# Kernel optimization log

Measured on AMD Instinct MI355X. Metric: run time of the kernel, lower is better.

## Reference

```python
import jax, jax.numpy as jnp
import numpy as np

PAD_LABEL = 15
NUM_TAGS = 15


def setup_inputs() -> dict:
    key = jax.random.key(0)
    k1, k2, k3 = jax.random.split(key, 3)
    B, T, C = 4096, 512, NUM_TAGS
    logits = jax.random.normal(k1, (B, T, C), dtype=jnp.float32)
    y_true = jax.random.randint(k2, (B, T), 0, PAD_LABEL + 1, dtype=jnp.int32)
    # CRF transition matrix (learned param), glorot-ish scale
    transitions = jax.random.normal(k3, (C, C), dtype=jnp.float32) * 0.25
    return {"logits": logits, "y_true": y_true, "transitions": transitions}


def _log_norm(logits, transitions, mask):
    # logits: (B, T, C) float32, mask: (B, T) bool
    alpha0 = logits[:, 0, :]                       # (B, C)
    # scan over timesteps 1..T-1
    emits = jnp.swapaxes(logits[:, 1:, :], 0, 1)    # (T-1, B, C)
    masks = jnp.swapaxes(mask[:, 1:], 0, 1)         # (T-1, B)

    def step(alpha, inp):
        emit_t, mask_t = inp                        # (B, C), (B,)
        # scores[b, i, j] = alpha[b, i] + trans[i, j] + emit_t[b, j]
        scores = alpha[:, :, None] + transitions[None, :, :] + emit_t[:, None, :]
        new_alpha = jax.scipy.special.logsumexp(scores, axis=1)  # (B, C)
        alpha = jnp.where(mask_t[:, None], new_alpha, alpha)
        return alpha, None

    alpha, _ = jax.lax.scan(step, alpha0, (emits, masks))
    return jax.scipy.special.logsumexp(alpha, axis=1)  # (B,)


def _sequence_score(logits, transitions, labels, mask):
    mask_f = mask.astype(jnp.float32)
    safe_labels = jnp.where(mask, labels, 0)                    # (B, T)
    # emission scores along gold path
    em = jnp.take_along_axis(logits, safe_labels[:, :, None], axis=2)[:, :, 0]
    emission_score = jnp.sum(em * mask_f, axis=1)               # (B,)
    # transition scores between consecutive valid positions
    prev, curr = safe_labels[:, :-1], safe_labels[:, 1:]
    tmask_f = (mask[:, 1:] & mask[:, :-1]).astype(jnp.float32)
    trans_scores = transitions[prev, curr]                      # (B, T-1)
    transition_score = jnp.sum(trans_scores * tmask_f, axis=1)  # (B,)
    return emission_score + transition_score


def reference(logits, y_true, transitions):
    mask = y_true != PAD_LABEL                                  # (B, T) bool
    logZ = _log_norm(logits, transitions, mask)
    path_score = _sequence_score(logits, transitions, y_true, mask)
    nll = jnp.clip(logZ - path_score, 0.0, 1000000.0)
    return jnp.mean(nll)
```

## Files before the change

kernel.cpp:

```cpp
#include <hip/hip_runtime.h>

#define L2E  1.4426950408889634f
#define LN2f 0.6931471805599453f

template<int CTRL>
__device__ __forceinline__ float dppf(float x) {
  int r = __builtin_amdgcn_update_dpp(0, __builtin_bit_cast(int, x), CTRL, 0xF, 0xF, true);
  return __builtin_bit_cast(float, r);
}
template<int CTRL>
__device__ __forceinline__ int dppi(int x) {
  return __builtin_amdgcn_update_dpp(0, x, CTRL, 0xF, 0xF, true);
}

__device__ __forceinline__ float bflymax16(float x) {
  x = fmaxf(x, dppf<0xB1>(x));
  x = fmaxf(x, dppf<0x4E>(x));
  x = fmaxf(x, dppf<0x141>(x));
  x = fmaxf(x, dppf<0x140>(x));
  return x;
}

#define DOT(shv, tot) {                                   \
    float t0_ = (shv) * Wror[0], t1_ = 0.f, t2_ = 0.f, t3_ = 0.f; \
    t1_ = fmaf(dppf<0x121>(shv), Wror[1],  t1_);          \
    t2_ = fmaf(dppf<0x122>(shv), Wror[2],  t2_);          \
    t3_ = fmaf(dppf<0x123>(shv), Wror[3],  t3_);          \
    t0_ = fmaf(dppf<0x124>(shv), Wror[4],  t0_);          \
    t1_ = fmaf(dppf<0x125>(shv), Wror[5],  t1_);          \
    t2_ = fmaf(dppf<0x126>(shv), Wror[6],  t2_);          \
    t3_ = fmaf(dppf<0x127>(shv), Wror[7],  t3_);          \
    t0_ = fmaf(dppf<0x128>(shv), Wror[8],  t0_);          \
    t1_ = fmaf(dppf<0x129>(shv), Wror[9],  t1_);          \
    t2_ = fmaf(dppf<0x12A>(shv), Wror[10], t2_);          \
    t3_ = fmaf(dppf<0x12B>(shv), Wror[11], t3_);          \
    t0_ = fmaf(dppf<0x12C>(shv), Wror[12], t0_);          \
    t1_ = fmaf(dppf<0x12D>(shv), Wror[13], t1_);          \
    t2_ = fmaf(dppf<0x12E>(shv), Wror[14], t2_);          \
    t3_ = fmaf(dppf<0x12F>(shv), Wror[15], t3_);          \
    tot = (t0_ + t1_) + (t2_ + t3_); }

template<bool BWD>
__device__ __forceinline__ void scan(const float* __restrict__ ep,
                                     const int* __restrict__ ys,
                                     const float (&Wror)[16],
                                     int j, int jm,
                                     float& ownO, float& MO, float& eaccO) {
  float own, M, eacc;
  float ebuf[8]; int ybuf[8];
  if (!BWD) {
    const float a0 = ep[0];
    const int y0 = ys[0];
    eacc = (y0 == jm) ? a0 : 0.f;
    const float A = (j < 15) ? a0 * L2E : -1.0e30f;
    const float M0 = bflymax16(A);
    own = exp2f(A - M0);
    M = M0;
    #pragma unroll
    for (int i = 0; i < 8; ++i) { ebuf[i] = ep[(1 + i) * 15]; ybuf[i] = ys[1 + i]; }
  } else {
    eacc = 0.f;
    own = (j < 15) ? 1.f : 0.f;
    M = 0.f;
    #pragma unroll
    for (int i = 0; i < 8; ++i) { ebuf[i] = ep[(511 - i) * 15]; ybuf[i] = ys[511 - i]; }
  }

  if (!BWD) {
    for (int sb = 0; sb < 31; ++sb) {
      #pragma unroll
      for (int k = 0; k < 8; ++k) {
        const int t = 1 + sb * 8 + k;
        const float emit = ebuf[k]; const int yv = ybuf[k];
        const int tn = (t + 8 > 255) ? 255 : t + 8;
        ebuf[k] = ep[tn * 15]; ybuf[k] = ys[tn];
        const float p = exp2f(emit * L2E);
        float tot; DOT(own, tot);
        const float cand = tot * p;
        own = (yv != 15) ? cand : own;
        eacc += (yv == jm) ? emit : 0.f;
        if (k == 7) {
          const float m = bflymax16(own);
          own *= __builtin_amdgcn_rcpf(m);
          M += log2f(m);
        }
      }
    }
    #pragma unroll
    for (int k = 0; k < 7; ++k) {
      const float emit = ebuf[k]; const int yv = ybuf[k];
      const float p = exp2f(emit * L2E);
      float tot; DOT(own, tot);
      const float cand = tot * p;
      own = (yv != 15) ? cand : own;
      eacc += (yv == jm) ? emit : 0.f;
    }
  } else {
    for (int sb = 0; sb < 32; ++sb) {
      #pragma unroll
      for (int k = 0; k < 8; ++k) {
        const int t = 511 - (sb * 8 + k);
        const float emit = ebuf[k]; const int yv = ybuf[k];
        const int tn = (t - 8 < 256) ? 256 : t - 8;
        ebuf[k] = ep[tn * 15]; ybuf[k] = ys[tn];
        const float p = exp2f(emit * L2E);
        const float share = own * p;
        float tot; DOT(share, tot);
        own = (yv != 15) ? tot : own;
        eacc += (yv == jm) ? emit : 0.f;
        if (k == 7) {
          const float m = bflymax16(own);
          own *= __builtin_amdgcn_rcpf(m);
          M += log2f(m);
        }
      }
    }
  }
  ownO = own; MO = M; eaccO = eacc;
}

__global__ __launch_bounds__(256, 2)
void crf_rot(const float* __restrict__ logits, const int* __restrict__ yg,
             const float* __restrict__ trans, float* __restrict__ out) {
  __shared__ float Tl[240];
  __shared__ int   yl[8 * 512];
  __shared__ float comb[8][2][16];
  __shared__ float pathE[8][2];
  __shared__ float transS[8];
  __shared__ float blks[8];

  const int tid = threadIdx.x;
  if (tid < 225) Tl[tid] = trans[tid];
  {
    const int4* src = (const int4*)(yg + (size_t)blockIdx.x * 4096);
    int4* dst = (int4*)yl;
    #pragma unroll
    for (int k = 0; k < 4; ++k) dst[tid + k * 256] = src[tid + k * 256];
  }
  __syncthreads();

  {
    const int q = tid >> 5, l32 = tid & 31;
    const int* ys = yl + q * 512;
    float acc = 0.f;
    #pragma unroll
    for (int m = 0; m < 16; ++m) {
      const int t = 1 + l32 + 32 * m;
      if (t < 512) {
        const int yc = ys[t], yp = ys[t - 1];
        if (yc < 15 && yp < 15) acc += Tl[yp * 15 + yc];
      }
    }
    #pragma unroll
    for (int k = 1; k < 32; k <<= 1) acc += __shfl_xor(acc, k, 32);
    if (l32 == 0) transS[q] = acc;
  }

  const int wave = tid >> 6, lane = tid & 63;
  const int j = lane & 15;
  const int sLoc = (wave >> 1) * 4 + (lane >> 4);
  const bool isFwd = (wave & 1) == 0;
  const int seq = blockIdx.x * 8 + sLoc;
  const int jj = (j < 15) ? j : 14;
  const int jm = (j < 15) ? j : 255;
  const float* ep = logits + (size_t)seq * 7680 + jj;
  const int* ys = yl + sLoc * 512;

  float Wror[16];
  Wror[0] = (j < 15) ? exp2f(Tl[j * 16] * L2E) : 0.f;
#define SETW(R) { const int s_ = dppi<0x120 + (R)>(j);                  \
    const bool v_ = (j < 15) && (s_ < 15);                              \
    const int ix_ = isFwd ? s_ * 15 + j : j * 15 + s_;                  \
    Wror[R] = v_ ? exp2f(Tl[ix_] * L2E) : 0.f; }
  SETW(1)  SETW(2)  SETW(3)  SETW(4)  SETW(5)
  SETW(6)  SETW(7)  SETW(8)  SETW(9)  SETW(10)
  SETW(11) SETW(12) SETW(13) SETW(14) SETW(15)
#undef SETW

  float own, M, eacc;
  if (isFwd) scan<false>(ep, ys, Wror, j, jm, own, M, eacc);
  else       scan<true >(ep, ys, Wror, j, jm, own, M, eacc);

  const int dir = isFwd ? 0 : 1;
  if (j < 15) comb[sLoc][dir][j] = M + log2f(own);
  #pragma unroll
  for (int k = 1; k < 16; k <<= 1) eacc += __shfl_xor(eacc, k, 16);
  if (j == 0) pathE[sLoc][dir] = eacc;

  __syncthreads();

  if (tid < 8) {
    float mx = -3.0e38f; float s[15];
    #pragma unroll
    for (int i = 0; i < 15; ++i) {
      s[i] = comb[tid][0][i] + comb[tid][1][i];
      mx = fmaxf(mx, s[i]);
    }
    float sum = 0.f;
    #pragma unroll
    for (int i = 0; i < 15; ++i) sum += exp2f(s[i] - mx);
    const float logZ = (mx + log2f(sum)) * LN2f;
    const float path = pathE[tid][0] + pathE[tid][1] + transS[tid];
    float nll = logZ - path;
    nll = fminf(fmaxf(nll, 0.f), 1000000.f);
    blks[tid] = nll;
  }
  __syncthreads();
  if (tid == 0) {
    float tot = (blks[0] + blks[1]) + (blks[2] + blks[3]) +
                (blks[4] + blks[5]) + (blks[6] + blks[7]);
    atomicAdd(out, tot * (1.0f / 4096.0f));
  }
}

extern "C" void kernel_launch(void* const* d_in, const int* in_sizes, int n_in,
                              void* d_out, int out_size, void* d_ws, size_t ws_size,
                              hipStream_t stream) {
  const float* logits = (const float*)d_in[0];
  const int*   y      = (const int*)d_in[1];
  const float* trans  = (const float*)d_in[2];
  float* out = (float*)d_out;

  hipMemsetAsync(out, 0, sizeof(float), stream);

  const int B = in_sizes[1] / 512;
  crf_rot<<<dim3(B / 8), dim3(256), 0, stream>>>(logits, y, trans, out);
}
```

Before: 68.44 us.

## Run CRF forward/backward recursion as bf16 MFMA matrix-vector products

Replaces the per-lane DPP rotation dot product with a 16x16x16 bf16 MFMA per timestep, so each wave handles one sequence direction and block size drops from 8 to 2 sequences. Renormalisation now happens every 4 steps using the first lane's value instead of every 8 steps with a butterfly max. Launch bounds move to 8 blocks per CU. The recurrence state is rounded to bf16 each step, which risks accuracy loss, and the serial MFMA latency on the dependency chain may dominate.

```diff
diff --git a/kernel.cpp b/kernel.cpp
--- a/kernel.cpp
+++ b/kernel.cpp
@@ -1,216 +1,236 @@
 #include <hip/hip_runtime.h>
+#include <hip/hip_bf16.h>
 
 #define L2E  1.4426950408889634f
 #define LN2f 0.6931471805599453f
 
-template<int CTRL>
-__device__ __forceinline__ float dppf(float x) {
-  int r = __builtin_amdgcn_update_dpp(0, __builtin_bit_cast(int, x), CTRL, 0xF, 0xF, true);
-  return __builtin_bit_cast(float, r);
-}
-template<int CTRL>
-__device__ __forceinline__ int dppi(int x) {
-  return __builtin_amdgcn_update_dpp(0, x, CTRL, 0xF, 0xF, true);
-}
-
-__device__ __forceinline__ float bflymax16(float x) {
-  x = fmaxf(x, dppf<0xB1>(x));
-  x = fmaxf(x, dppf<0x4E>(x));
-  x = fmaxf(x, dppf<0x141>(x));
-  x = fmaxf(x, dppf<0x140>(x));
-  return x;
-}
-
-#define DOT(shv, tot) {                                   \
-    float t0_ = (shv) * Wror[0], t1_ = 0.f, t2_ = 0.f, t3_ = 0.f; \
-    t1_ = fmaf(dppf<0x121>(shv), Wror[1],  t1_);          \
-    t2_ = fmaf(dppf<0x122>(shv), Wror[2],  t2_);          \
-    t3_ = fmaf(dppf<0x123>(shv), Wror[3],  t3_);          \
-    t0_ = fmaf(dppf<0x124>(shv), Wror[4],  t0_);          \
-    t1_ = fmaf(dppf<0x125>(shv), Wror[5],  t1_);          \
-    t2_ = fmaf(dppf<0x126>(shv), Wror[6],  t2_);          \
-    t3_ = fmaf(dppf<0x127>(shv), Wror[7],  t3_);          \
-    t0_ = fmaf(dppf<0x128>(shv), Wror[8],  t0_);          \
-    t1_ = fmaf(dppf<0x129>(shv), Wror[9],  t1_);          \
-    t2_ = fmaf(dppf<0x12A>(shv), Wror[10], t2_);          \
-    t3_ = fmaf(dppf<0x12B>(shv), Wror[11], t3_);          \
-    t0_ = fmaf(dppf<0x12C>(shv), Wror[12], t0_);          \
-    t1_ = fmaf(dppf<0x12D>(shv), Wror[13], t1_);          \
-    t2_ = fmaf(dppf<0x12E>(shv), Wror[14], t2_);          \
-    t3_ = fmaf(dppf<0x12F>(shv), Wror[15], t3_);          \
-    tot = (t0_ + t1_) + (t2_ + t3_); }
+typedef __attribute__((ext_vector_type(4))) float f32x4;
+typedef __attribute__((ext_vector_type(4))) short s16x4;
+
+#if __has_builtin(__builtin_amdgcn_mfma_f32_16x16x16bf16_1k)
+__device__ __forceinline__ f32x4 mfma16(s16x4 a, s16x4 b) {
+  f32x4 z = {0.f, 0.f, 0.f, 0.f};
+  return __builtin_amdgcn_mfma_f32_16x16x16bf16_1k(a, b, z, 0, 0, 0);
+}
+#else
+__device__ __forceinline__ f32x4 mfma16(s16x4 a, s16x4 b) {
+  f32x4 d = {0.f, 0.f, 0.f, 0.f};
+  asm volatile("s_nop 1\n\t"
+               "v_mfma_f32_16x16x16_bf16 %0, %1, %2, %0\n\t"
+               "s_nop 7\n\ts_nop 7"
+               : "+v"(d) : "v"(a), "v"(b));
+  return d;
+}
+#endif
+
+__device__ __forceinline__ short f2bf(float f) {
+  __hip_bfloat16 h = __float2bfloat16(f);
+  return (short)__builtin_bit_cast(unsigned short, h);
+}
+__device__ __forceinline__ float rfl(float v) {
+  return __builtin_bit_cast(float,
+      __builtin_amdgcn_readfirstlane(__builtin_bit_cast(int, v)));
+}
 
 template<bool BWD>
-__device__ __forceinline__ void scan(const float* __restrict__ ep,
-                                     const int* __restrict__ ys,
-                                     const float (&Wror)[16],
-                                     int j, int jm,
-                                     float& ownO, float& MO, float& eaccO) {
-  float own, M, eacc;
-  float ebuf[8]; int ybuf[8];
+__device__ __forceinline__ void scan_mfma(
+    const float* __restrict__ ep,
+    const int*   __restrict__ ys,
+    const float (&Wf)[4], const float (&If)[4], const s16x4 Ibf,
+    int r, int jj, int g4, int lane,
+    float* __restrict__ comb16, float* __restrict__ aux2)
+{
+  const int jm = (r < 15) ? r : 255;
+  const bool isCol0 = (r == 0);
+
+  const float* e0 = BWD ? (ep + 511 * 15) : ep;
+  float dv[4];
+  #pragma unroll
+  for (int q = 0; q < 4; ++q) {
+    const int rowq = g4 * 4 + q;
+    const float ev = e0[(rowq < 15) ? rowq : 14];
+    dv[q] = (isCol0 && rowq < 15) ? ev : 0.0f;
+  }
+  const float base = rfl(dv[0]);
+  float M = base * L2E;
+  s16x4 b16;
+  #pragma unroll
+  for (int q = 0; q < 4; ++q) {
+    const int rowq = g4 * 4 + q;
+    const float x = (isCol0 && rowq < 15) ? exp2f((dv[q] - base) * L2E) : 0.0f;
+    dv[q] = x;
+    b16[q] = f2bf(x);
+  }
+
+  const float* erow = ep + jj;
+  float ering[8]; int ybuf[8];
+  float eacc, ecur = 0.f, pcur = 1.f;
+  const float* pe; const int* py;
   if (!BWD) {
-    const float a0 = ep[0];
+    #pragma unroll
+    for (int i = 0; i < 8; ++i) { ering[i] = erow[(1 + i) * 15]; ybuf[i] = ys[1 + i]; }
+    pe = erow + 9 * 15;  py = ys + 9;
     const int y0 = ys[0];
-    eacc = (y0 == jm) ? a0 : 0.f;
-    const float A = (j < 15) ? a0 * L2E : -1.0e30f;
-    const float M0 = bflymax16(A);
-    own = exp2f(A - M0);
-    M = M0;
-    #pragma unroll
-    for (int i = 0; i < 8; ++i) { ebuf[i] = ep[(1 + i) * 15]; ybuf[i] = ys[1 + i]; }
+    eacc = (y0 == jm) ? erow[0] : 0.f;
   } else {
+    #pragma unroll
+    for (int i = 0; i < 8; ++i) { ering[i] = erow[(510 - i) * 15]; ybuf[i] = ys[511 - i]; }
+    pe = erow + 502 * 15;  py = ys + 503;
+    ecur = erow[511 * 15];
+    pcur = exp2f(ecur * L2E);
     eacc = 0.f;
-    own = (j < 15) ? 1.f : 0.f;
-    M = 0.f;
-    #pragma unroll
-    for (int i = 0; i < 8; ++i) { ebuf[i] = ep[(511 - i) * 15]; ybuf[i] = ys[511 - i]; }
-  }
+  }
+
+  f32x4 d;
+
+#define STEP(kk, RN)                                                        \
+  do {                                                                      \
+    const float ev_ = ering[kk]; const int yv_ = ybuf[kk];                  \
+    ering[kk] = *pe; ybuf[kk] = *py;                                        \
+    if (!BWD) { pe += 15; py += 1; } else { pe -= 15; py -= 1; }            \
+    const bool mk_ = (yv_ != 15);                                           \
+    const float pn_ = exp2f(ev_ * L2E);                                     \
+    s16x4 a16_;                                                             \
+    if (!BWD) {                                                             \
+      a16_[0] = f2bf(pn_ * Wf[0]); a16_[1] = f2bf(pn_ * Wf[1]);             \
+      a16_[2] = f2bf(pn_ * Wf[2]); a16_[3] = f2bf(pn_ * Wf[3]);             \
+      if (!mk_) a16_ = Ibf;                                                 \
+      eacc += (yv_ == jm) ? ev_ : 0.f;                                      \
+    } else {                                                                \
+      const float rr_ = pn_ * __builtin_amdgcn_rcpf(pcur);                  \
+      a16_[0] = f2bf(mk_ ? pn_ * Wf[0] : rr_ * If[0]);                      \
+      a16_[1] = f2bf(mk_ ? pn_ * Wf[1] : rr_ * If[1]);                      \
+      a16_[2] = f2bf(mk_ ? pn_ * Wf[2] : rr_ * If[2]);                      \
+      a16_[3] = f2bf(mk_ ? pn_ * Wf[3] : rr_ * If[3]);                      \
+      eacc += (yv_ == jm) ? ecur : 0.f;                                     \
+      ecur = ev_; pcur = pn_;                                               \
+    }                                                                       \
+    d = mfma16(a16_, b16);                                                  \
+    if (RN) {                                                               \
+      const float m_ = rfl(d[0]);                                           \
+      M += log2f(m_);                                                       \
+      const float iv_ = __builtin_amdgcn_rcpf(m_);                          \
+      d[0] *= iv_; d[1] *= iv_; d[2] *= iv_; d[3] *= iv_;                   \
+    }                                                                       \
+    b16[0] = f2bf(d[0]); b16[1] = f2bf(d[1]);                               \
+    b16[2] = f2bf(d[2]); b16[3] = f2bf(d[3]);                               \
+  } while (0)
 
   if (!BWD) {
     for (int sb = 0; sb < 31; ++sb) {
-      #pragma unroll
-      for (int k = 0; k < 8; ++k) {
-        const int t = 1 + sb * 8 + k;
-        const float emit = ebuf[k]; const int yv = ybuf[k];
-        const int tn = (t + 8 > 255) ? 255 : t + 8;
-        ebuf[k] = ep[tn * 15]; ybuf[k] = ys[tn];
-        const float p = exp2f(emit * L2E);
-        float tot; DOT(own, tot);
-        const float cand = tot * p;
-        own = (yv != 15) ? cand : own;
-        eacc += (yv == jm) ? emit : 0.f;
-        if (k == 7) {
-          const float m = bflymax16(own);
-          own *= __builtin_amdgcn_rcpf(m);
-          M += log2f(m);
-        }
-      }
-    }
-    #pragma unroll
-    for (int k = 0; k < 7; ++k) {
-      const float emit = ebuf[k]; const int yv = ybuf[k];
-      const float p = exp2f(emit * L2E);
-      float tot; DOT(own, tot);
-      const float cand = tot * p;
-      own = (yv != 15) ? cand : own;
-      eacc += (yv == jm) ? emit : 0.f;
-    }
+      STEP(0, 0); STEP(1, 0); STEP(2, 0); STEP(3, 1);
+      STEP(4, 0); STEP(5, 0); STEP(6, 0); STEP(7, 1);
+    }
+    STEP(0, 0); STEP(1, 0); STEP(2, 0); STEP(3, 1);
+    STEP(4, 0); STEP(5, 0); STEP(6, 0);
   } else {
     for (int sb = 0; sb < 32; ++sb) {
-      #pragma unroll
-      for (int k = 0; k < 8; ++k) {
-        const int t = 511 - (sb * 8 + k);
-        const float emit = ebuf[k]; const int yv = ybuf[k];
-        const int tn = (t - 8 < 256) ? 256 : t - 8;
-        ebuf[k] = ep[tn * 15]; ybuf[k] = ys[tn];
-        const float p = exp2f(emit * L2E);
-        const float share = own * p;
-        float tot; DOT(share, tot);
-        own = (yv != 15) ? tot : own;
-        eacc += (yv == jm) ? emit : 0.f;
-        if (k == 7) {
-          const float m = bflymax16(own);
-          own *= __builtin_amdgcn_rcpf(m);
-          M += log2f(m);
-        }
-      }
-    }
-  }
-  ownO = own; MO = M; eaccO = eacc;
-}
-
-__global__ __launch_bounds__(256, 2)
-void crf_rot(const float* __restrict__ logits, const int* __restrict__ yg,
-             const float* __restrict__ trans, float* __restrict__ out) {
+      STEP(0, 0); STEP(1, 0); STEP(2, 0); STEP(3, 1);
+      STEP(4, 0); STEP(5, 0); STEP(6, 0); STEP(7, 1);
+    }
+  }
+#undef STEP
+
+  if (isCol0) {
+    #pragma unroll
+    for (int q = 0; q < 4; ++q) {
+      const float x = d[q];
+      comb16[g4 * 4 + q] = (x > 0.f) ? (M + log2f(x)) : -1.0e30f;
+    }
+  }
+  eacc += __shfl_xor(eacc, 1, 16);
+  eacc += __shfl_xor(eacc, 2, 16);
+  eacc += __shfl_xor(eacc, 4, 16);
+  eacc += __shfl_xor(eacc, 8, 16);
+  if (lane == 0) aux2[0] = eacc;
+}
+
+__global__ __launch_bounds__(256, 8)
+void crf_mfma2(const float* __restrict__ logits, const int* __restrict__ yg,
+               const float* __restrict__ trans, float* __restrict__ out) {
   __shared__ float Tl[240];
-  __shared__ int   yl[8 * 512];
-  __shared__ float comb[8][2][16];
-  __shared__ float pathE[8][2];
-  __shared__ float transS[8];
-  __shared__ float blks[8];
+  __shared__ int   yl[1024];
+  __shared__ float comb[2][2][16];
+  __shared__ float emS[2][2];
+  __shared__ float transS[2];
+  __shared__ float blks[2];
 
   const int tid = threadIdx.x;
   if (tid < 225) Tl[tid] = trans[tid];
+  if (tid < 2) transS[tid] = 0.f;
+  ((int4*)yl)[tid] = ((const int4*)(yg + (size_t)blockIdx.x * 1024))[tid];
+  __syncthreads();
+
   {
-    const int4* src = (const int4*)(yg + (size_t)blockIdx.x * 4096);
-    int4* dst = (int4*)yl;
-    #pragma unroll
-    for (int k = 0; k < 4; ++k) dst[tid + k * 256] = src[tid + k * 256];
-  }
-  __syncthreads();
-
-  {
-    const int q = tid >> 5, l32 = tid & 31;
-    const int* ys = yl + q * 512;
+    const int q = tid >> 7, l = tid & 127;
+    const int* ysq = yl + q * 512;
     float acc = 0.f;
     #pragma unroll
-    for (int m = 0; m < 16; ++m) {
-      const int t = 1 + l32 + 32 * m;
+    for (int m = 0; m < 4; ++m) {
+      const int t = 1 + l + 128 * m;
       if (t < 512) {
-        const int yc = ys[t], yp = ys[t - 1];
+        const int yc = ysq[t], yp = ysq[t - 1];
         if (yc < 15 && yp < 15) acc += Tl[yp * 15 + yc];
       }
     }
     #pragma unroll
-    for (int k = 1; k < 32; k <<= 1) acc += __shfl_xor(acc, k, 32);
-    if (l32 == 0) transS[q] = acc;
+    for (int k = 1; k < 64; k <<= 1) acc += __shfl_xor(acc, k, 64);
+    if ((tid & 63) == 0) atomicAdd(&transS[q], acc);
   }
 
   const int wave = tid >> 6, lane = tid & 63;
-  const int j = lane & 15;
-  const int sLoc = (wave >> 1) * 4 + (lane >> 4);
-  const bool isFwd = (wave & 1) == 0;
-  const int seq = blockIdx.x * 8 + sLoc;
-  const int jj = (j < 15) ? j : 14;
-  const int jm = (j < 15) ? j : 255;
-  const float* ep = logits + (size_t)seq * 7680 + jj;
-  const int* ys = yl + sLoc * 512;
-
-  float Wror[16];
-  Wror[0] = (j < 15) ? exp2f(Tl[j * 16] * L2E) : 0.f;
-#define SETW(R) { const int s_ = dppi<0x120 + (R)>(j);                  \
-    const bool v_ = (j < 15) && (s_ < 15);                              \
-    const int ix_ = isFwd ? s_ * 15 + j : j * 15 + s_;                  \
-    Wror[R] = v_ ? exp2f(Tl[ix_] * L2E) : 0.f; }
-  SETW(1)  SETW(2)  SETW(3)  SETW(4)  SETW(5)
-  SETW(6)  SETW(7)  SETW(8)  SETW(9)  SETW(10)
-  SETW(11) SETW(12) SETW(13) SETW(14) SETW(15)
-#undef SETW
-
-  float own, M, eacc;
-  if (isFwd) scan<false>(ep, ys, Wror, j, jm, own, M, eacc);
-  else       scan<true >(ep, ys, Wror, j, jm, own, M, eacc);
-
-  const int dir = isFwd ? 0 : 1;
-  if (j < 15) comb[sLoc][dir][j] = M + log2f(own);
-  #pragma unroll
-  for (int k = 1; k < 16; k <<= 1) eacc += __shfl_xor(eacc, k, 16);
-  if (j == 0) pathE[sLoc][dir] = eacc;
+  const int sl = wave >> 1;
+  const bool isBwd = (wave & 1) != 0;
+  const int seq = blockIdx.x * 2 + sl;
+  const int r  = lane & 15;
+  const int jj = (r < 15) ? r : 14;
+  const int g4 = lane >> 4;
+
+  float Wf[4], If[4];
+  s16x4 Ibf;
+  #pragma unroll
+  for (int q = 0; q < 4; ++q) {
+    const int c = g4 * 4 + q;
+    const bool valid = (r < 15) && (c < 15);
+    const int idx = isBwd ? (r * 15 + c) : (c * 15 + r);
+    Wf[q] = valid ? exp2f(Tl[valid ? idx : 0] * L2E) : 0.f;
+    If[q] = (r == c) ? 1.f : 0.f;
+    Ibf[q] = f2bf(If[q]);
+  }
+  #pragma unroll
+  for (int q = 0; q < 4; ++q) asm volatile("" : "+v"(Wf[q]));
+
+  const float* ep = logits + (size_t)seq * 7680;
+  const int* ys = yl + sl * 512;
+  const int dir = isBwd ? 1 : 0;
+
+  if (isBwd) scan_mfma<true >(ep, ys, Wf, If, Ibf, r, jj, g4, lane,
+                              &comb[sl][1][0], &emS[sl][1]);
+  else       scan_mfma<false>(ep, ys, Wf, If, Ibf, r, jj, g4, lane,
+                              &comb[sl][0][0], &emS[sl][0]);
+  (void)dir;
 
   __syncthreads();
 
-  if (tid < 8) {
-    float mx = -3.0e38f; float s[15];
+  if (tid < 2) {
+    const float* e255 = logits + (size_t)(blockIdx.x * 2 + tid) * 7680 + 255 * 15;
+    float s[15]; float mx = -3.0e38f;
     #pragma unroll
     for (int i = 0; i < 15; ++i) {
-      s[i] = comb[tid][0][i] + comb[tid][1][i];
+      s[i] = comb[tid][0][i] + comb[tid][1][i] - e255[i] * L2E;
       mx = fmaxf(mx, s[i]);
     }
     float sum = 0.f;
     #pragma unroll
     for (int i = 0; i < 15; ++i) sum += exp2f(s[i] - mx);
     const float logZ = (mx + log2f(sum)) * LN2f;
-    const float path = pathE[tid][0] + pathE[tid][1] + transS[tid];
+    const float path = emS[tid][0] + emS[tid][1] + transS[tid];
     float nll = logZ - path;
     nll = fminf(fmaxf(nll, 0.f), 1000000.f);
     blks[tid] = nll;
   }
   __syncthreads();
-  if (tid == 0) {
-    float tot = (blks[0] + blks[1]) + (blks[2] + blks[3]) +
-                (blks[4] + blks[5]) + (blks[6] + blks[7]);
-    atomicAdd(out, tot * (1.0f / 4096.0f));
-  }
+  if (tid == 0) atomicAdd(out, (blks[0] + blks[1]) * (1.0f / 4096.0f));
 }
 
 extern "C" void kernel_launch(void* const* d_in, const int* in_sizes, int n_in,
@@ -224,5 +244,5 @@
   hipMemsetAsync(out, 0, sizeof(float), stream);
 
   const int B = in_sizes[1] / 512;
-  crf_rot<<<dim3(B / 8), dim3(256), 0, stream>>>(logits, y, trans, out);
-}
+  crf_mfma2<<<dim3(B / 2), dim3(256), 0, stream>>>(logits, y, trans, out);
+}
```

Result: slower. 150.9 us (+120.5%).

## Deepen register prefetch to 16 steps and read labels directly from global

Applied to the files above, without the earlier changes.

The prefetch ring for emissions and labels grows from 8 to 16 entries, giving each load more time to arrive before the scan step that uses it. The labels are no longer staged in LDS; each step reads them straight from global memory through byte-offset pointers that advance by a fixed stride, which removes the clamped index math. An asm barrier pins the transition weights in VGPRs. In exchange the kernel issues more outstanding global loads per thread, and the larger buffers raise register pressure, which could hurt occupancy under the 2-blocks launch bound.

```diff
diff --git a/kernel.cpp b/kernel.cpp
--- a/kernel.cpp
+++ b/kernel.cpp
@@ -40,90 +40,103 @@
     t3_ = fmaf(dppf<0x12F>(shv), Wror[15], t3_);          \
     tot = (t0_ + t1_) + (t2_ + t3_); }
 
+#define STEPF(kk, RN, REFILL)                                         \
+  do {                                                                \
+    const float emit = ebuf[kk]; const int yi = ybuf[kk];             \
+    if (REFILL) {                                                     \
+      ebuf[kk] = *(const float*)(lb + eoff); eoff += 60;              \
+      ybuf[kk] = *(const int*)(yb + yoff); yoff += 4;                 \
+    }                                                                 \
+    const float p = exp2f(emit * L2E);                                \
+    float tot; DOT(own, tot);                                         \
+    const float cand = tot * p;                                       \
+    own = (yi != 15) ? cand : own;                                    \
+    eacc += (yi == jm) ? emit : 0.f;                                  \
+    if (RN) { const float m = bflymax16(own);                         \
+      own *= __builtin_amdgcn_rcpf(m); M += log2f(m); }               \
+  } while (0)
+
+#define STEPB(kk, RN, REFILL)                                         \
+  do {                                                                \
+    const float emit = ebuf[kk]; const int yi = ybuf[kk];             \
+    if (REFILL) {                                                     \
+      ebuf[kk] = *(const float*)(lb + eoff); eoff -= 60;              \
+      ybuf[kk] = *(const int*)(yb + yoff); yoff -= 4;                 \
+    }                                                                 \
+    const float p = exp2f(emit * L2E);                                \
+    const float share = own * p;                                      \
+    float tot; DOT(share, tot);                                       \
+    own = (yi != 15) ? tot : own;                                     \
+    eacc += (yi == jm) ? emit : 0.f;                                  \
+    if (RN) { const float m = bflymax16(own);                         \
+      own *= __builtin_amdgcn_rcpf(m); M += log2f(m); }               \
+  } while (0)
+
 template<bool BWD>
-__device__ __forceinline__ void scan(const float* __restrict__ ep,
-                                     const int* __restrict__ ys,
+__device__ __forceinline__ void scan(const char* __restrict__ lb,
+                                     const char* __restrict__ yb,
                                      const float (&Wror)[16],
                                      int j, int jm,
                                      float& ownO, float& MO, float& eaccO) {
   float own, M, eacc;
-  float ebuf[8]; int ybuf[8];
+  float ebuf[16]; int ybuf[16];
+  int eoff, yoff;
   if (!BWD) {
-    const float a0 = ep[0];
-    const int y0 = ys[0];
+    const float a0 = *(const float*)lb;
+    const int y0 = *(const int*)yb;
     eacc = (y0 == jm) ? a0 : 0.f;
     const float A = (j < 15) ? a0 * L2E : -1.0e30f;
     const float M0 = bflymax16(A);
     own = exp2f(A - M0);
     M = M0;
     #pragma unroll
-    for (int i = 0; i < 8; ++i) { ebuf[i] = ep[(1 + i) * 15]; ybuf[i] = ys[1 + i]; }
+    for (int i = 0; i < 16; ++i) {
+      ebuf[i] = *(const float*)(lb + (1 + i) * 60);
+      ybuf[i] = *(const int*)(yb + (1 + i) * 4);
+    }
+    eoff = 17 * 60; yoff = 17 * 4;
   } else {
     eacc = 0.f;
     own = (j < 15) ? 1.f : 0.f;
     M = 0.f;
     #pragma unroll
-    for (int i = 0; i < 8; ++i) { ebuf[i] = ep[(511 - i) * 15]; ybuf[i] = ys[511 - i]; }
+    for (int i = 0; i < 16; ++i) {
+      ebuf[i] = *(const float*)(lb + (511 - i) * 60);
+      ybuf[i] = *(const int*)(yb + (511 - i) * 4);
+    }
+    eoff = 495 * 60; yoff = 495 * 4;
   }
 
   if (!BWD) {
-    for (int sb = 0; sb < 31; ++sb) {
-      #pragma unroll
-      for (int k = 0; k < 8; ++k) {
-        const int t = 1 + sb * 8 + k;
-        const float emit = ebuf[k]; const int yv = ybuf[k];
-        const int tn = (t + 8 > 255) ? 255 : t + 8;
-        ebuf[k] = ep[tn * 15]; ybuf[k] = ys[tn];
-        const float p = exp2f(emit * L2E);
-        float tot; DOT(own, tot);
-        const float cand = tot * p;
-        own = (yv != 15) ? cand : own;
-        eacc += (yv == jm) ? emit : 0.f;
-        if (k == 7) {
-          const float m = bflymax16(own);
-          own *= __builtin_amdgcn_rcpf(m);
-          M += log2f(m);
-        }
-      }
-    }
-    #pragma unroll
-    for (int k = 0; k < 7; ++k) {
-      const float emit = ebuf[k]; const int yv = ybuf[k];
-      const float p = exp2f(emit * L2E);
-      float tot; DOT(own, tot);
-      const float cand = tot * p;
-      own = (yv != 15) ? cand : own;
-      eacc += (yv == jm) ? emit : 0.f;
-    }
+    for (int sb = 0; sb < 15; ++sb) {
+      STEPF(0,0,1);  STEPF(1,0,1);  STEPF(2,0,1);  STEPF(3,0,1);
+      STEPF(4,0,1);  STEPF(5,0,1);  STEPF(6,0,1);  STEPF(7,1,1);
+      STEPF(8,0,1);  STEPF(9,0,1);  STEPF(10,0,1); STEPF(11,0,1);
+      STEPF(12,0,1); STEPF(13,0,1); STEPF(14,0,1); STEPF(15,1,1);
+    }
+    STEPF(0,0,0);  STEPF(1,0,0);  STEPF(2,0,0);  STEPF(3,0,0);
+    STEPF(4,0,0);  STEPF(5,0,0);  STEPF(6,0,0);  STEPF(7,1,0);
+    STEPF(8,0,0);  STEPF(9,0,0);  STEPF(10,0,0); STEPF(11,0,0);
+    STEPF(12,0,0); STEPF(13,0,0); STEPF(14,0,0);
   } else {
-    for (int sb = 0; sb < 32; ++sb) {
-      #pragma unroll
-      for (int k = 0; k < 8; ++k) {
-        const int t = 511 - (sb * 8 + k);
-        const float emit = ebuf[k]; const int yv = ybuf[k];
-        const int tn = (t - 8 < 256) ? 256 : t - 8;
-        ebuf[k] = ep[tn * 15]; ybuf[k] = ys[tn];
-        const float p = exp2f(emit * L2E);
-        const float share = own * p;
-        float tot; DOT(share, tot);
-        own = (yv != 15) ? tot : own;
-        eacc += (yv == jm) ? emit : 0.f;
-        if (k == 7) {
-          const float m = bflymax16(own);
-          own *= __builtin_amdgcn_rcpf(m);
-          M += log2f(m);
-        }
-      }
-    }
+    for (int sb = 0; sb < 15; ++sb) {
+      STEPB(0,0,1);  STEPB(1,0,1);  STEPB(2,0,1);  STEPB(3,0,1);
+      STEPB(4,0,1);  STEPB(5,0,1);  STEPB(6,0,1);  STEPB(7,1,1);
+      STEPB(8,0,1);  STEPB(9,0,1);  STEPB(10,0,1); STEPB(11,0,1);
+      STEPB(12,0,1); STEPB(13,0,1); STEPB(14,0,1); STEPB(15,1,1);
+    }
+    STEPB(0,0,0);  STEPB(1,0,0);  STEPB(2,0,0);  STEPB(3,0,0);
+    STEPB(4,0,0);  STEPB(5,0,0);  STEPB(6,0,0);  STEPB(7,1,0);
+    STEPB(8,0,0);  STEPB(9,0,0);  STEPB(10,0,0); STEPB(11,0,0);
+    STEPB(12,0,0); STEPB(13,0,0); STEPB(14,0,0); STEPB(15,0,0);
   }
   ownO = own; MO = M; eaccO = eacc;
 }
 
 __global__ __launch_bounds__(256, 2)
-void crf_rot(const float* __restrict__ logits, const int* __restrict__ yg,
-             const float* __restrict__ trans, float* __restrict__ out) {
+void crf_g(const float* __restrict__ logits, const int* __restrict__ yg,
+           const float* __restrict__ trans, float* __restrict__ out) {
   __shared__ float Tl[240];
-  __shared__ int   yl[8 * 512];
   __shared__ float comb[8][2][16];
   __shared__ float pathE[8][2];
   __shared__ float transS[8];
@@ -131,17 +144,13 @@
 
   const int tid = threadIdx.x;
   if (tid < 225) Tl[tid] = trans[tid];
-  {
-    const int4* src = (const int4*)(yg + (size_t)blockIdx.x * 4096);
-    int4* dst = (int4*)yl;
-    #pragma unroll
-    for (int k = 0; k < 4; ++k) dst[tid + k * 256] = src[tid + k * 256];
-  }
   __syncthreads();
+
+  const char* yb0 = (const char*)yg + (size_t)blockIdx.x * 8 * 2048;
 
   {
     const int q = tid >> 5, l32 = tid & 31;
-    const int* ys = yl + q * 512;
+    const int* ys = (const int*)(yb0 + q * 2048);
     float acc = 0.f;
     #pragma unroll
     for (int m = 0; m < 16; ++m) {
@@ -163,23 +172,25 @@
   const int seq = blockIdx.x * 8 + sLoc;
   const int jj = (j < 15) ? j : 14;
   const int jm = (j < 15) ? j : 255;
-  const float* ep = logits + (size_t)seq * 7680 + jj;
-  const int* ys = yl + sLoc * 512;
+  const char* lb = (const char*)logits + (size_t)seq * 30720 + jj * 4;
+  const char* yb = yb0 + sLoc * 2048;
 
   float Wror[16];
   Wror[0] = (j < 15) ? exp2f(Tl[j * 16] * L2E) : 0.f;
 #define SETW(R) { const int s_ = dppi<0x120 + (R)>(j);                  \
     const bool v_ = (j < 15) && (s_ < 15);                              \
     const int ix_ = isFwd ? s_ * 15 + j : j * 15 + s_;                  \
-    Wror[R] = v_ ? exp2f(Tl[ix_] * L2E) : 0.f; }
+    Wror[R] = v_ ? exp2f(Tl[v_ ? ix_ : 0] * L2E) : 0.f; }
   SETW(1)  SETW(2)  SETW(3)  SETW(4)  SETW(5)
   SETW(6)  SETW(7)  SETW(8)  SETW(9)  SETW(10)
   SETW(11) SETW(12) SETW(13) SETW(14) SETW(15)
 #undef SETW
+  #pragma unroll
+  for (int r = 0; r < 16; ++r) asm volatile("" : "+v"(Wror[r]));
 
   float own, M, eacc;
-  if (isFwd) scan<false>(ep, ys, Wror, j, jm, own, M, eacc);
-  else       scan<true >(ep, ys, Wror, j, jm, own, M, eacc);
+  if (isFwd) scan<false>(lb, yb, Wror, j, jm, own, M, eacc);
+  else       scan<true >(lb, yb, Wror, j, jm, own, M, eacc);
 
   const int dir = isFwd ? 0 : 1;
   if (j < 15) comb[sLoc][dir][j] = M + log2f(own);
@@ -207,8 +218,8 @@
   }
   __syncthreads();
   if (tid == 0) {
-    float tot = (blks[0] + blks[1]) + (blks[2] + blks[3]) +
-                (blks[4] + blks[5]) + (blks[6] + blks[7]);
+    const float tot = (blks[0] + blks[1]) + (blks[2] + blks[3]) +
+                      (blks[4] + blks[5]) + (blks[6] + blks[7]);
     atomicAdd(out, tot * (1.0f / 4096.0f));
   }
 }
@@ -224,5 +235,5 @@
   hipMemsetAsync(out, 0, sizeof(float), stream);
 
   const int B = in_sizes[1] / 512;
-  crf_rot<<<dim3(B / 8), dim3(256), 0, stream>>>(logits, y, trans, out);
-}
+  crf_g<<<dim3(B / 8), dim3(256), 0, stream>>>(logits, y, trans, out);
+}
```

Result: faster. 63.49 us (-7.2%).

## Replace DPP rotation dot product with bf16 MFMA matrix-vector per timestep

Applied to the files above, without the earlier changes.

Each wave now computes the CRF forward/backward recurrence as a 16x16x16 bf16 MFMA, with the exp-transition matrix held as the A operand and the state of 4 sequences as the B operand. This replaces the 16 DPP-shuffled FMAs per step. Emissions are read as unaligned float4 loads straight from global memory, and labels are read directly from global rather than staged in LDS. The cost is that state rounds to bf16 every step, which loses accuracy, and each step now waits on MFMA latency inside a serial dependency chain.

```diff
diff --git a/kernel.cpp b/kernel.cpp
--- a/kernel.cpp
+++ b/kernel.cpp
@@ -1,129 +1,128 @@
 #include <hip/hip_runtime.h>
+#include <hip/hip_bf16.h>
 
 #define L2E  1.4426950408889634f
 #define LN2f 0.6931471805599453f
 
-template<int CTRL>
-__device__ __forceinline__ float dppf(float x) {
-  int r = __builtin_amdgcn_update_dpp(0, __builtin_bit_cast(int, x), CTRL, 0xF, 0xF, true);
-  return __builtin_bit_cast(float, r);
-}
-template<int CTRL>
-__device__ __forceinline__ int dppi(int x) {
-  return __builtin_amdgcn_update_dpp(0, x, CTRL, 0xF, 0xF, true);
-}
-
-__device__ __forceinline__ float bflymax16(float x) {
-  x = fmaxf(x, dppf<0xB1>(x));
-  x = fmaxf(x, dppf<0x4E>(x));
-  x = fmaxf(x, dppf<0x141>(x));
-  x = fmaxf(x, dppf<0x140>(x));
-  return x;
-}
-
-#define DOT(shv, tot) {                                   \
-    float t0_ = (shv) * Wror[0], t1_ = 0.f, t2_ = 0.f, t3_ = 0.f; \
-    t1_ = fmaf(dppf<0x121>(shv), Wror[1],  t1_);          \
-    t2_ = fmaf(dppf<0x122>(shv), Wror[2],  t2_);          \
-    t3_ = fmaf(dppf<0x123>(shv), Wror[3],  t3_);          \
-    t0_ = fmaf(dppf<0x124>(shv), Wror[4],  t0_);          \
-    t1_ = fmaf(dppf<0x125>(shv), Wror[5],  t1_);          \
-    t2_ = fmaf(dppf<0x126>(shv), Wror[6],  t2_);          \
-    t3_ = fmaf(dppf<0x127>(shv), Wror[7],  t3_);          \
-    t0_ = fmaf(dppf<0x128>(shv), Wror[8],  t0_);          \
-    t1_ = fmaf(dppf<0x129>(shv), Wror[9],  t1_);          \
-    t2_ = fmaf(dppf<0x12A>(shv), Wror[10], t2_);          \
-    t3_ = fmaf(dppf<0x12B>(shv), Wror[11], t3_);          \
-    t0_ = fmaf(dppf<0x12C>(shv), Wror[12], t0_);          \
-    t1_ = fmaf(dppf<0x12D>(shv), Wror[13], t1_);          \
-    t2_ = fmaf(dppf<0x12E>(shv), Wror[14], t2_);          \
-    t3_ = fmaf(dppf<0x12F>(shv), Wror[15], t3_);          \
-    tot = (t0_ + t1_) + (t2_ + t3_); }
-
-template<bool BWD>
-__device__ __forceinline__ void scan(const float* __restrict__ ep,
-                                     const int* __restrict__ ys,
-                                     const float (&Wror)[16],
-                                     int j, int jm,
-                                     float& ownO, float& MO, float& eaccO) {
-  float own, M, eacc;
-  float ebuf[8]; int ybuf[8];
-  if (!BWD) {
-    const float a0 = ep[0];
-    const int y0 = ys[0];
-    eacc = (y0 == jm) ? a0 : 0.f;
-    const float A = (j < 15) ? a0 * L2E : -1.0e30f;
-    const float M0 = bflymax16(A);
-    own = exp2f(A - M0);
-    M = M0;
-    #pragma unroll
-    for (int i = 0; i < 8; ++i) { ebuf[i] = ep[(1 + i) * 15]; ybuf[i] = ys[1 + i]; }
-  } else {
-    eacc = 0.f;
-    own = (j < 15) ? 1.f : 0.f;
-    M = 0.f;
-    #pragma unroll
-    for (int i = 0; i < 8; ++i) { ebuf[i] = ep[(511 - i) * 15]; ybuf[i] = ys[511 - i]; }
-  }
-
-  if (!BWD) {
-    for (int sb = 0; sb < 31; ++sb) {
-      #pragma unroll
-      for (int k = 0; k < 8; ++k) {
-        const int t = 1 + sb * 8 + k;
-        const float emit = ebuf[k]; const int yv = ybuf[k];
-        const int tn = (t + 8 > 255) ? 255 : t + 8;
-        ebuf[k] = ep[tn * 15]; ybuf[k] = ys[tn];
-        const float p = exp2f(emit * L2E);
-        float tot; DOT(own, tot);
-        const float cand = tot * p;
-        own = (yv != 15) ? cand : own;
-        eacc += (yv == jm) ? emit : 0.f;
-        if (k == 7) {
-          const float m = bflymax16(own);
-          own *= __builtin_amdgcn_rcpf(m);
-          M += log2f(m);
-        }
-      }
-    }
-    #pragma unroll
-    for (int k = 0; k < 7; ++k) {
-      const float emit = ebuf[k]; const int yv = ybuf[k];
-      const float p = exp2f(emit * L2E);
-      float tot; DOT(own, tot);
-      const float cand = tot * p;
-      own = (yv != 15) ? cand : own;
-      eacc += (yv == jm) ? emit : 0.f;
-    }
-  } else {
-    for (int sb = 0; sb < 32; ++sb) {
-      #pragma unroll
-      for (int k = 0; k < 8; ++k) {
-        const int t = 511 - (sb * 8 + k);
-        const float emit = ebuf[k]; const int yv = ybuf[k];
-        const int tn = (t - 8 < 256) ? 256 : t - 8;
-        ebuf[k] = ep[tn * 15]; ybuf[k] = ys[tn];
-        const float p = exp2f(emit * L2E);
-        const float share = own * p;
-        float tot; DOT(share, tot);
-        own = (yv != 15) ? tot : own;
-        eacc += (yv == jm) ? emit : 0.f;
-        if (k == 7) {
-          const float m = bflymax16(own);
-          own *= __builtin_amdgcn_rcpf(m);
-          M += log2f(m);
-        }
-      }
-    }
-  }
-  ownO = own; MO = M; eaccO = eacc;
-}
+typedef __attribute__((ext_vector_type(4))) float f32x4;
+typedef __attribute__((ext_vector_type(4), aligned(4))) float f32x4u;
+typedef __attribute__((ext_vector_type(4))) short s16x4;
+
+#if __has_builtin(__builtin_amdgcn_mfma_f32_16x16x16bf16_1k)
+__device__ __forceinline__ f32x4 mfma16(s16x4 a, s16x4 b) {
+  f32x4 z = {0.f, 0.f, 0.f, 0.f};
+  return __builtin_amdgcn_mfma_f32_16x16x16bf16_1k(a, b, z, 0, 0, 0);
+}
+#else
+__device__ __forceinline__ f32x4 mfma16(s16x4 a, s16x4 b) {
+  f32x4 d = {0.f, 0.f, 0.f, 0.f};
+  asm volatile("s_nop 1\n\t"
+               "v_mfma_f32_16x16x16_bf16 %0, %1, %2, %0\n\t"
+               "s_nop 7\n\ts_nop 7"
+               : "+v"(d) : "v"(a), "v"(b));
+  return d;
+}
+#endif
+
+__device__ __forceinline__ short f2bf(float f) {
+  __hip_bfloat16 h = __float2bfloat16(f);
+  return (short)__builtin_bit_cast(unsigned short, h);
+}
+
+#define YSELF(TL) ( ((TL)&3)==0 ? (((TL)&4)? yq1.x : yq0.x) : \
+                    ((TL)&3)==1 ? (((TL)&4)? yq1.y : yq0.y) : \
+                    ((TL)&3)==2 ? (((TL)&4)? yq1.z : yq0.z) : \
+                                  (((TL)&4)? yq1.w : yq0.w) )
+#define YSELB(TL) ( ((TL)&3)==0 ? (((TL)&4)? yq0.w : yq1.w) : \
+                    ((TL)&3)==1 ? (((TL)&4)? yq0.z : yq1.z) : \
+                    ((TL)&3)==2 ? (((TL)&4)? yq0.y : yq1.y) : \
+                                  (((TL)&4)? yq0.x : yq1.x) )
+
+#define STEPF(TL) do { \
+    const f32x4 e4_ = ering[(TL) & 7]; \
+    ering[(TL) & 7] = *(const f32x4u*)(ebc + ((TL) + 8) * 60); \
+    const int yv_ = YSELF(TL); \
+    const float u0_ = sel3 ? e4_.y : e4_.x; \
+    const float u1_ = sel3 ? e4_.z : e4_.y; \
+    const float u2_ = sel3 ? e4_.w : e4_.z; \
+    const float u3_ = e4_.w; \
+    const f32x4 dd_ = mfma16(af, b16); \
+    const float p0_ = exp2f(u0_ * L2E), p1_ = exp2f(u1_ * L2E); \
+    const float p2_ = exp2f(u2_ * L2E), p3_ = exp2f(u3_ * L2E); \
+    const bool mk_ = (yv_ != 15); \
+    st0 = mk_ ? dd_[0] * p0_ : st0; \
+    st1 = mk_ ? dd_[1] * p1_ : st1; \
+    st2 = mk_ ? dd_[2] * p2_ : st2; \
+    st3 = mk_ ? dd_[3] * p3_ : st3; \
+    const float v01_ = (yv_ & 1) ? u1_ : u0_; \
+    const float v23_ = (yv_ & 1) ? u3_ : u2_; \
+    const float vv_ = (yv_ & 2) ? v23_ : v01_; \
+    eacc += (mk_ & ((yv_ >> 2) == g4)) ? vv_ : 0.f; \
+    if (((TL) & 7) == 7) { \
+      yq0 = *(const int4*)(ybc + ((TL) + 1) * 4); \
+      yq1 = *(const int4*)(ybc + ((TL) + 5) * 4); \
+      float mx_ = fmaxf(fmaxf(st0, st1), fmaxf(st2, st3)); \
+      mx_ = fmaxf(mx_, __shfl_xor(mx_, 16, 64)); \
+      mx_ = fmaxf(mx_, __shfl_xor(mx_, 32, 64)); \
+      const float rs_ = __builtin_amdgcn_rcpf(mx_); \
+      st0 *= rs_; st1 *= rs_; st2 *= rs_; st3 *= rs_; \
+      M += log2f(mx_); \
+    } \
+    b16[0] = f2bf(st0); b16[1] = f2bf(st1); \
+    b16[2] = f2bf(st2); b16[3] = f2bf(st3); \
+  } while (0)
+
+#define STEPB(TL) do { \
+    const f32x4 e4_ = ering[7 - ((TL) & 7)]; \
+    ering[7 - ((TL) & 7)] = *(const f32x4u*)(ebc - ((TL) + 8) * 60); \
+    const int yv_ = YSELB(TL); \
+    const float u0_ = sel3 ? e4_.y : e4_.x; \
+    const float u1_ = sel3 ? e4_.z : e4_.y; \
+    const float u2_ = sel3 ? e4_.w : e4_.z; \
+    const float u3_ = e4_.w; \
+    const float p0_ = exp2f(u0_ * L2E), p1_ = exp2f(u1_ * L2E); \
+    const float p2_ = exp2f(u2_ * L2E), p3_ = exp2f(u3_ * L2E); \
+    b16[0] = f2bf(st0 * p0_); b16[1] = f2bf(st1 * p1_); \
+    b16[2] = f2bf(st2 * p2_); b16[3] = f2bf(st3 * p3_); \
+    const f32x4 dd_ = mfma16(af, b16); \
+    const bool mk_ = (yv_ != 15); \
+    st0 = mk_ ? dd_[0] : st0; \
+    st1 = mk_ ? dd_[1] : st1; \
+    st2 = mk_ ? dd_[2] : st2; \
+    st3 = mk_ ? dd_[3] : st3; \
+    const float v01_ = (yv_ & 1) ? u1_ : u0_; \
+    const float v23_ = (yv_ & 1) ? u3_ : u2_; \
+    const float vv_ = (yv_ & 2) ? v23_ : v01_; \
+    eacc += (mk_ & ((yv_ >> 2) == g4)) ? vv_ : 0.f; \
+    if (((TL) & 7) == 7) { \
+      yq0 = *(const int4*)(ybc - ((TL) + 8) * 4); \
+      yq1 = *(const int4*)(ybc - ((TL) + 4) * 4); \
+      float mx_ = fmaxf(fmaxf(st0, st1), fmaxf(st2, st3)); \
+      mx_ = fmaxf(mx_, __shfl_xor(mx_, 16, 64)); \
+      mx_ = fmaxf(mx_, __shfl_xor(mx_, 32, 64)); \
+      const float rs_ = __builtin_amdgcn_rcpf(mx_); \
+      st0 *= rs_; st1 *= rs_; st2 *= rs_; st3 *= rs_; \
+      M += log2f(mx_); \
+    } \
+  } while (0)
+
+#define FB32_ { STEPF(0); STEPF(1); STEPF(2); STEPF(3); STEPF(4); STEPF(5); STEPF(6); STEPF(7); \
+                STEPF(8); STEPF(9); STEPF(10); STEPF(11); STEPF(12); STEPF(13); STEPF(14); STEPF(15); \
+                STEPF(16); STEPF(17); STEPF(18); STEPF(19); STEPF(20); STEPF(21); STEPF(22); STEPF(23); \
+                STEPF(24); STEPF(25); STEPF(26); STEPF(27); STEPF(28); STEPF(29); STEPF(30); STEPF(31); }
+#define FB31_ { STEPF(1); STEPF(2); STEPF(3); STEPF(4); STEPF(5); STEPF(6); STEPF(7); \
+                STEPF(8); STEPF(9); STEPF(10); STEPF(11); STEPF(12); STEPF(13); STEPF(14); STEPF(15); \
+                STEPF(16); STEPF(17); STEPF(18); STEPF(19); STEPF(20); STEPF(21); STEPF(22); STEPF(23); \
+                STEPF(24); STEPF(25); STEPF(26); STEPF(27); STEPF(28); STEPF(29); STEPF(30); STEPF(31); }
+#define BB32_ { STEPB(0); STEPB(1); STEPB(2); STEPB(3); STEPB(4); STEPB(5); STEPB(6); STEPB(7); \
+                STEPB(8); STEPB(9); STEPB(10); STEPB(11); STEPB(12); STEPB(13); STEPB(14); STEPB(15); \
+                STEPB(16); STEPB(17); STEPB(18); STEPB(19); STEPB(20); STEPB(21); STEPB(22); STEPB(23); \
+                STEPB(24); STEPB(25); STEPB(26); STEPB(27); STEPB(28); STEPB(29); STEPB(30); STEPB(31); }
 
 __global__ __launch_bounds__(256, 2)
-void crf_rot(const float* __restrict__ logits, const int* __restrict__ yg,
+void crf_mm4(const float* __restrict__ logits, const int* __restrict__ yg,
              const float* __restrict__ trans, float* __restrict__ out) {
   __shared__ float Tl[240];
-  __shared__ int   yl[8 * 512];
   __shared__ float comb[8][2][16];
   __shared__ float pathE[8][2];
   __shared__ float transS[8];
@@ -131,17 +130,13 @@
 
   const int tid = threadIdx.x;
   if (tid < 225) Tl[tid] = trans[tid];
-  {
-    const int4* src = (const int4*)(yg + (size_t)blockIdx.x * 4096);
-    int4* dst = (int4*)yl;
-    #pragma unroll
-    for (int k = 0; k < 4; ++k) dst[tid + k * 256] = src[tid + k * 256];
-  }
   __syncthreads();
+
+  const char* yub0 = (const char*)yg + (size_t)blockIdx.x * (8 * 2048);
 
   {
     const int q = tid >> 5, l32 = tid & 31;
-    const int* ys = yl + q * 512;
+    const int* ys = (const int*)(yub0 + q * 2048);
     float acc = 0.f;
     #pragma unroll
     for (int m = 0; m < 16; ++m) {
@@ -156,36 +151,107 @@
     if (l32 == 0) transS[q] = acc;
   }
 
-  const int wave = tid >> 6, lane = tid & 63;
-  const int j = lane & 15;
-  const int sLoc = (wave >> 1) * 4 + (lane >> 4);
-  const bool isFwd = (wave & 1) == 0;
-  const int seq = blockIdx.x * 8 + sLoc;
-  const int jj = (j < 15) ? j : 14;
-  const int jm = (j < 15) ? j : 255;
-  const float* ep = logits + (size_t)seq * 7680 + jj;
-  const int* ys = yl + sLoc * 512;
-
-  float Wror[16];
-  Wror[0] = (j < 15) ? exp2f(Tl[j * 16] * L2E) : 0.f;
-#define SETW(R) { const int s_ = dppi<0x120 + (R)>(j);                  \
-    const bool v_ = (j < 15) && (s_ < 15);                              \
-    const int ix_ = isFwd ? s_ * 15 + j : j * 15 + s_;                  \
-    Wror[R] = v_ ? exp2f(Tl[ix_] * L2E) : 0.f; }
-  SETW(1)  SETW(2)  SETW(3)  SETW(4)  SETW(5)
-  SETW(6)  SETW(7)  SETW(8)  SETW(9)  SETW(10)
-  SETW(11) SETW(12) SETW(13) SETW(14) SETW(15)
-#undef SETW
-
-  float own, M, eacc;
-  if (isFwd) scan<false>(ep, ys, Wror, j, jm, own, M, eacc);
-  else       scan<true >(ep, ys, Wror, j, jm, own, M, eacc);
-
+  const int wv = tid >> 6, lane = tid & 63;
+  const int c  = lane & 15;
+  const int g4 = lane >> 4;
+  const int r0 = g4 * 4;
+  const bool sel3 = (g4 == 3);
+  const int cc = (c < 4) ? c : 3;
+  const int grp = wv >> 1;
+  const bool isFwd = (wv & 1) == 0;
   const int dir = isFwd ? 0 : 1;
-  if (j < 15) comb[sLoc][dir][j] = M + log2f(own);
-  #pragma unroll
-  for (int k = 1; k < 16; k <<= 1) eacc += __shfl_xor(eacc, k, 16);
-  if (j == 0) pathE[sLoc][dir] = eacc;
+  const size_t seq = (size_t)(blockIdx.x * 8 + grp * 4 + cc);
+  const int off4 = sel3 ? 44 : r0 * 4;
+
+  const char* ebc = (const char*)logits + seq * 30720 + off4;
+  const char* ybc = (const char*)yg + seq * 2048;
+
+  int2 afi;
+  {
+    short as0, as1, as2, as3;
+    short* asp[4] = {&as0, &as1, &as2, &as3};
+    #pragma unroll
+    for (int q = 0; q < 4; ++q) {
+      const int k = r0 + q;
+      const bool valid = (c < 15) && (k < 15);
+      const int idx = isFwd ? (k * 15 + c) : (c * 15 + k);
+      *asp[q] = f2bf(valid ? exp2f(Tl[valid ? idx : 0] * L2E) : 0.f);
+    }
+    afi.x = (int)(unsigned short)as0 | ((int)(unsigned short)as1 << 16);
+    afi.y = (int)(unsigned short)as2 | ((int)(unsigned short)as3 << 16);
+  }
+  asm volatile("" : "+v"(afi.x), "+v"(afi.y));
+  const s16x4 af = __builtin_bit_cast(s16x4, afi);
+
+  f32x4 ering[8];
+  int4 yq0, yq1;
+  s16x4 b16;
+  float st0, st1, st2, st3, M, eacc;
+
+  if (isFwd) {
+    ering[1] = *(const f32x4u*)(ebc + 60);
+    ering[2] = *(const f32x4u*)(ebc + 120);
+    ering[3] = *(const f32x4u*)(ebc + 180);
+    ering[4] = *(const f32x4u*)(ebc + 240);
+    ering[5] = *(const f32x4u*)(ebc + 300);
+    ering[6] = *(const f32x4u*)(ebc + 360);
+    ering[7] = *(const f32x4u*)(ebc + 420);
+    ering[0] = *(const f32x4u*)(ebc + 480);
+    yq0 = *(const int4*)(ybc);
+    yq1 = *(const int4*)(ybc + 16);
+    const f32x4 ez = *(const f32x4u*)(ebc);
+    const float u0_ = sel3 ? ez.y : ez.x;
+    const float u1_ = sel3 ? ez.z : ez.y;
+    const float u2_ = sel3 ? ez.w : ez.z;
+    const float u3_ = ez.w;
+    float mx_ = fmaxf(fmaxf(u0_, u1_), fmaxf(u2_, sel3 ? u2_ : u3_));
+    mx_ = fmaxf(mx_, __shfl_xor(mx_, 16, 64));
+    mx_ = fmaxf(mx_, __shfl_xor(mx_, 32, 64));
+    st0 = exp2f((u0_ - mx_) * L2E);
+    st1 = exp2f((u1_ - mx_) * L2E);
+    st2 = exp2f((u2_ - mx_) * L2E);
+    st3 = sel3 ? 0.f : exp2f((u3_ - mx_) * L2E);
+    M = mx_ * L2E;
+    b16[0] = f2bf(st0); b16[1] = f2bf(st1); b16[2] = f2bf(st2); b16[3] = f2bf(st3);
+    const int y0_ = yq0.x;
+    const bool mk0 = (y0_ != 15);
+    const float v01_ = (y0_ & 1) ? u1_ : u0_;
+    const float v23_ = (y0_ & 1) ? u3_ : u2_;
+    const float vv_ = (y0_ & 2) ? v23_ : v01_;
+    eacc = (mk0 & ((y0_ >> 2) == g4)) ? vv_ : 0.f;
+
+    FB31_;
+    #pragma unroll 1
+    for (int b = 0; b < 7; ++b) { ebc += 1920; ybc += 128; FB32_; }
+  } else {
+    ebc += 511 * 60;
+    ybc += 511 * 4;
+    ering[7] = *(const f32x4u*)(ebc);
+    ering[6] = *(const f32x4u*)(ebc - 60);
+    ering[5] = *(const f32x4u*)(ebc - 120);
+    ering[4] = *(const f32x4u*)(ebc - 180);
+    ering[3] = *(const f32x4u*)(ebc - 240);
+    ering[2] = *(const f32x4u*)(ebc - 300);
+    ering[1] = *(const f32x4u*)(ebc - 360);
+    ering[0] = *(const f32x4u*)(ebc - 420);
+    yq0 = *(const int4*)(ybc - 28);
+    yq1 = *(const int4*)(ybc - 12);
+    st0 = 1.f; st1 = 1.f; st2 = 1.f; st3 = sel3 ? 0.f : 1.f;
+    M = 0.f; eacc = 0.f;
+    #pragma unroll 1
+    for (int b = 0; b < 8; ++b) { BB32_; ebc -= 1920; ybc -= 128; }
+  }
+
+  if (c < 4) {
+    float* cb = &comb[grp * 4 + c][dir][0];
+    cb[r0 + 0] = M + log2f(st0);
+    cb[r0 + 1] = M + log2f(st1);
+    cb[r0 + 2] = M + log2f(st2);
+    if (!sel3) cb[r0 + 3] = M + log2f(st3);
+  }
+  eacc += __shfl_xor(eacc, 16, 64);
+  eacc += __shfl_xor(eacc, 32, 64);
+  if (c < 4 && g4 == 0) pathE[grp * 4 + c][dir] = eacc;
 
   __syncthreads();
 
@@ -207,8 +273,8 @@
   }
   __syncthreads();
   if (tid == 0) {
-    float tot = (blks[0] + blks[1]) + (blks[2] + blks[3]) +
-                (blks[4] + blks[5]) + (blks[6] + blks[7]);
+    const float tot = (blks[0] + blks[1]) + (blks[2] + blks[3]) +
+                      (blks[4] + blks[5]) + (blks[6] + blks[7]);
     atomicAdd(out, tot * (1.0f / 4096.0f));
   }
 }
@@ -224,5 +290,5 @@
   hipMemsetAsync(out, 0, sizeof(float), stream);
 
   const int B = in_sizes[1] / 512;
-  crf_rot<<<dim3(B / 8), dim3(256), 0, stream>>>(logits, y, trans, out);
-}
+  crf_mm4<<<dim3(B / 8), dim3(256), 0, stream>>>(logits, y, trans, out);
+}
```

After: 89.86 us. +31.3%, slower.
